# Kernel optimization log

Measured on AMD Instinct MI355X. Metric: run time of the kernel, lower is better.

The kernel has to match this reference:

```python
import jax, jax.numpy as jnp
import numpy as np
from jax import lax

B, N, L, P, C, D = 64, 20000, 336, 96, 16, 64
COARSE_K, TOPM, ALPHA, TEMP = 80, 20, 0.7, 0.1
CAT_DIM, N_TAB, GH = 16, 17, 128
ID_MIN = np.array([0,0,0,0,0,1,1,0,0,0,0,0,0,0,0,0,0], dtype=np.int64)
ID_MAX = np.array([2047,255,4095,23,6,12,53,3,1,1,15,7,2,2,2,2,1], dtype=np.int64)

def _gelu(x):
    return jax.nn.gelu(x, approximate=False)

def _mlp2(x, w1, b1, w2, b2):
    return _gelu(x @ w1 + b1) @ w2 + b2

def _ln(x, g, b):
    m = x.mean(-1, keepdims=True)
    v = jnp.var(x, axis=-1, keepdims=True)
    return (x - m) / jnp.sqrt(v + 1e-5) * g + b

def _unit(x):
    return x / (jnp.linalg.norm(x, axis=-1, keepdims=True) + 1e-12)

def setup_inputs():
    key = jax.random.key(0)
    ks = jax.random.split(key, 24)
    s = 0.02
    z = jnp.zeros
    return {
        'meta_ids': jax.random.randint(ks[0], (B, N_TAB), 0, 2),
        'exogenous_vars': jax.random.normal(ks[1], (B, 8)),
        'local_state_by_period': jax.random.normal(ks[2], (B, 3, 4)),
        'x': jax.random.normal(ks[3], (B, L, C)),
        'pool_context': jax.random.normal(ks[4], (N, D)),
        'pool_x': jax.random.normal(ks[5], (N, L, C)),
        'pool_y': jax.random.normal(ks[6], (N, P, C)),
        'emb_tables': jax.random.normal(ks[7], (N_TAB, 4096, CAT_DIM)) * s,
        'cat_w1': jax.random.normal(ks[8], (N_TAB * CAT_DIM, D)) * s, 'cat_b1': z((D,)),
        'cat_w2': jax.random.normal(ks[9], (D, D)) * s, 'cat_b2': z((D,)),
        'exo_w1': jax.random.normal(ks[10], (8, D)) * s, 'exo_b1': z((D,)),
        'exo_w2': jax.random.normal(ks[11], (D, D)) * s, 'exo_b2': z((D,)),
        'loc_w1': jax.random.normal(ks[12], (4, D)) * s, 'loc_b1': z((D,)),
        'loc_w2': jax.random.normal(ks[13], (D, D)) * s, 'loc_b2': z((D,)),
        'ln_g': jnp.ones((D,)), 'ln_b': z((D,)),
        'gate_w1': jax.random.normal(ks[14], (2 * D + 2, GH)) * s, 'gate_b1': z((GH,)),
        'gate_w2': jax.random.normal(ks[15], (GH, 1)) * s, 'gate_b2': z((1,)),
    }

def _forward(meta_ids, exogenous_vars, local_state_by_period, x, pool_context, pool_x, pool_y,
             emb_tables, cat_w1, cat_b1, cat_w2, cat_b2, exo_w1, exo_b1, exo_w2, exo_b2,
             loc_w1, loc_b1, loc_w2, loc_b2, ln_g, ln_b, gate_w1, gate_b1, gate_w2, gate_b2):
    # --- hierarchical context encoder ---
    ids = jnp.clip(meta_ids, jnp.asarray(ID_MIN)[None, :], jnp.asarray(ID_MAX)[None, :])
    # per-table embedding lookup -> [B, 17, cat_dim]
    cat = jax.vmap(lambda t, i: t[i], in_axes=(0, 1), out_axes=1)(emb_tables, ids)
    cat = cat.reshape(B, N_TAB * CAT_DIM)
    cat_ctx = _mlp2(cat, cat_w1, cat_b1, cat_w2, cat_b2)
    cat_ctx = cat_ctx + _mlp2(exogenous_vars, exo_w1, exo_b1, exo_w2, exo_b2)
    loc = _mlp2(local_state_by_period.reshape(-1, 4), loc_w1, loc_b1, loc_w2, loc_b2).reshape(B, 3, D)
    ctx = _ln(cat_ctx[:, None, :] + loc, ln_g, ln_b)       # [B, 3, D]
    q = ctx.mean(axis=1)                                    # pooled query context [B, D]
    # --- coarse retrieval: cosine sim over meta pool ---
    meta_sim = _unit(q) @ _unit(pool_context).T             # [B, N]
    meta_c, coarse_idx = lax.top_k(meta_sim, COARSE_K)      # [B, K]
    cand_ctx = pool_context[coarse_idx]                     # [B, K, D]
    cand_x = pool_x[coarse_idx]                             # [B, K, L, C]
    # --- fine similarity on raw series ---
    xf = _unit(x.reshape(B, L * C))
    cf = _unit(cand_x.reshape(B, COARSE_K, L * C))
    series_sim = jnp.einsum('bd,bkd->bk', xf, cf)
    combined = ALPHA * meta_c + (1.0 - ALPHA) * series_sim
    comb_m, li = lax.top_k(combined, TOPM)                  # [B, M]
    meta_m = jnp.take_along_axis(meta_c, li, axis=1)
    ctx_m = jnp.take_along_axis(cand_ctx, li[..., None], axis=1)   # [B, M, D]
    fin_idx = jnp.take_along_axis(coarse_idx, li, axis=1)
    cand_y = pool_y[fin_idx]                                # [B, M, P, C]
    # --- gated aggregation ---
    gate_in = jnp.concatenate([
        jnp.broadcast_to(q[:, None, :], (B, TOPM, D)), ctx_m,
        comb_m[..., None], meta_m[..., None]], axis=-1)     # [B, M, 2D+2]
    gate = _mlp2(gate_in, gate_w1, gate_b1, gate_w2, gate_b2)[..., 0]
    w = jax.nn.softmax(comb_m / TEMP + gate, axis=-1)       # [B, M]
    return jnp.einsum('bm,bmpc->bpc', w, cand_y)            # [B, P, C]

def reference(meta_ids, exogenous_vars, local_state_by_period, x, pool_context, pool_x, pool_y,
              emb_tables, cat_w1, cat_b1, cat_w2, cat_b2, exo_w1, exo_b1, exo_w2, exo_b2,
              loc_w1, loc_b1, loc_w2, loc_b2, ln_g, ln_b, gate_w1, gate_b1, gate_w2, gate_b2):
    return _forward(meta_ids, exogenous_vars, local_state_by_period, x, pool_context, pool_x, pool_y,
                    emb_tables, cat_w1, cat_b1, cat_w2, cat_b2, exo_w1, exo_b1, exo_w2, exo_b2,
                    loc_w1, loc_b1, loc_w2, loc_b2, ln_g, ln_b, gate_w1, gate_b1, gate_w2, gate_b2)
```

## Files before the change

kernel.cpp:

```cpp
#include <hip/hip_runtime.h>
#include <math.h>

typedef unsigned int u32;

#define BB 64
#define NN 20000
#define LL 336
#define PP 96
#define CC 16
#define DD 64
#define KC 80
#define TM 20
#define LC 5376
#define NTAB 17
#define GH 128
#define CAP 2048

__constant__ int c_idmin[17] = {0,0,0,0,0,1,1,0,0,0,0,0,0,0,0,0,0};
__constant__ int c_idmax[17] = {2047,255,4095,23,6,12,53,3,1,1,15,7,2,2,2,2,1};

__device__ __forceinline__ float gelu(float x){ return 0.5f*x*(1.0f + erff(x*0.70710678118654752440f)); }
__device__ __forceinline__ float wred(float v){
  #pragma unroll
  for(int m=32;m>=1;m>>=1) v += __shfl_xor(v, m, 64);
  return v;
}
__device__ __forceinline__ u32 fkey(float f){
  u32 u = __float_as_uint(f);
  return (u & 0x80000000u) ? ~u : (u | 0x80000000u);
}

#define OFF_Q     0u
#define OFF_QN    16384u
#define OFF_XN    32768u
#define OFF_CIDX  33024u
#define OFF_METC  53504u
#define OFF_COMB  73984u
#define OFF_FIDX  94464u
#define OFF_W     99584u
#define OFF_SIM   106496u

__global__ __launch_bounds__(64) void k_ctx(
    const int* __restrict__ mids, const float* __restrict__ exo,
    const float* __restrict__ locs, const float* __restrict__ x,
    const float* __restrict__ emb,
    const float* __restrict__ cw1, const float* __restrict__ cb1,
    const float* __restrict__ cw2, const float* __restrict__ cb2,
    const float* __restrict__ ew1, const float* __restrict__ eb1,
    const float* __restrict__ ew2, const float* __restrict__ eb2,
    const float* __restrict__ lw1, const float* __restrict__ lb1,
    const float* __restrict__ lw2, const float* __restrict__ lb2,
    const float* __restrict__ lng, const float* __restrict__ lnb,
    float* __restrict__ q, float* __restrict__ qn, float* __restrict__ xn)
{
  int b = blockIdx.x, j = threadIdx.x;
  __shared__ float s_cat[272];
  __shared__ float s_h[64];
  __shared__ float s_exo[8];
  __shared__ float s_loc[12];

  for(int e=j; e<272; e+=64){
    int t=e>>4, c=e&15;
    int id = mids[b*NTAB + t];
    if(id < c_idmin[t]) id = c_idmin[t];
    if(id > c_idmax[t]) id = c_idmax[t];
    s_cat[e] = emb[((size_t)t*4096 + id)*16 + c];
  }
  if(j<8)  s_exo[j] = exo[b*8+j];
  if(j<12) s_loc[j] = locs[b*12+j];
  __syncthreads();

  float a = cb1[j];
  for(int i=0;i<272;i++) a += s_cat[i]*cw1[i*64+j];
  s_h[j] = gelu(a);
  __syncthreads();
  float cc = cb2[j];
  for(int k=0;k<64;k++) cc += s_h[k]*cw2[k*64+j];
  __syncthreads();

  a = eb1[j];
  for(int i=0;i<8;i++) a += s_exo[i]*ew1[i*64+j];
  s_h[j] = gelu(a);
  __syncthreads();
  float ec = eb2[j];
  for(int k=0;k<64;k++) ec += s_h[k]*ew2[k*64+j];
  cc += ec;
  __syncthreads();

  float lr[3];
  for(int r=0;r<3;r++){
    a = lb1[j];
    for(int i=0;i<4;i++) a += s_loc[r*4+i]*lw1[i*64+j];
    s_h[j] = gelu(a);
    __syncthreads();
    float o = lb2[j];
    for(int k=0;k<64;k++) o += s_h[k]*lw2[k*64+j];
    lr[r] = o;
    __syncthreads();
  }

  float g = lng[j], be = lnb[j];
  float qa = 0.f;
  for(int r=0;r<3;r++){
    float v = cc + lr[r];
    float mean = wred(v) * (1.0f/64.0f);
    float d = v - mean;
    float var = wred(d*d) * (1.0f/64.0f);
    qa += d / sqrtf(var + 1e-5f) * g + be;
  }
  float qv = qa * (1.0f/3.0f);
  q[b*64+j] = qv;
  float s2 = wred(qv*qv);
  qn[b*64+j] = qv / (sqrtf(s2) + 1e-12f);

  float xa = 0.f;
  for(int e=j; e<LC; e+=64){ float f = x[(size_t)b*LC+e]; xa += f*f; }
  xa = wred(xa);
  if(j==0) xn[b] = sqrtf(xa);
}

__device__ __attribute__((noinline)) float row_sim(const float* pr, const float* sq)
{
  const float4* p4 = (const float4*)pr;
  float dot=0.f, ns=0.f;
  #pragma unroll
  for(int i=0;i<16;i++){
    float4 u = p4[i];
    dot += u.x*sq[i*4+0] + u.y*sq[i*4+1] + u.z*sq[i*4+2] + u.w*sq[i*4+3];
    ns  += u.x*u.x + u.y*u.y + u.z*u.z + u.w*u.w;
  }
  return dot / (sqrtf(ns) + 1e-12f);
}

__global__ __launch_bounds__(256) void k_sim(const float* __restrict__ pc,
    const float* __restrict__ qn, float* __restrict__ sim)
{
  __shared__ float s_pc[64*68];
  __shared__ float s_qn[4*64];
  int n0 = blockIdx.x << 6;
  int b0 = blockIdx.y << 2;
  int tid = threadIdx.x;

  const float4* pc4 = (const float4*)pc;
  for(int e=tid; e<64*16; e+=256){
    int r = e>>4, c = e&15;
    float4 v;
    if(n0 + r < NN) v = pc4[(size_t)(n0+r)*16 + c];
    else            v = make_float4(0.f,0.f,0.f,0.f);
    *(float4*)&s_pc[r*68 + c*4] = v;
  }
  s_qn[tid] = qn[(size_t)(b0 + (tid>>6))*64 + (tid&63)];
  __syncthreads();

  int bl = tid>>6, ln = tid&63;
  const float4* q4 = (const float4*)&s_qn[bl*64];
  const float4* p4 = (const float4*)&s_pc[ln*68];
  float dot=0.f, ns=0.f;
  #pragma unroll
  for(int i=0;i<16;i++){
    float4 p = p4[i], qv = q4[i];
    dot += p.x*qv.x + p.y*qv.y + p.z*qv.z + p.w*qv.w;
    ns  += p.x*p.x + p.y*p.y + p.z*p.z + p.w*p.w;
  }
  int n = n0 + ln;
  if(n < NN) sim[(size_t)(b0+bl)*NN + n] = dot / (sqrtf(ns) + 1e-12f);
}

__global__ __launch_bounds__(256) void k_sel(const float* __restrict__ sim,
    int* __restrict__ cidx_out, float* __restrict__ metc)
{
  __shared__ u32 hist[4096];
  __shared__ u32 cs[256];
  __shared__ float cval[CAP];
  __shared__ int  cidxs[CAP];
  __shared__ int s_T; __shared__ u32 s_above;
  __shared__ u32 s_na, s_nc;
  __shared__ float swv[4]; __shared__ int swi[4];
  int b = blockIdx.x, tid = threadIdx.x;
  const float* srow = sim + (size_t)b*NN;

  for(int e=tid;e<4096;e+=256) hist[e]=0;
  if(tid==0){ s_na=0; s_nc=0; }
  for(int e=tid;e<KC;e+=256){ cidx_out[b*KC+e]=0; metc[b*KC+e]=-1.0f; }
  __syncthreads();

  for(int n=tid;n<NN;n+=256) atomicAdd(&hist[fkey(srow[n])>>20], 1u);
  __syncthreads();
  u32 c=0;
  #pragma unroll
  for(int i=0;i<16;i++) c += hist[tid*16+i];
  cs[tid]=c;
  __syncthreads();
  if(tid==0){
    u32 acc=0, above=0; int T=0;
    for(int ch=255; ch>=0; --ch){
      if(acc + cs[ch] >= (u32)KC){
        for(int bin=ch*16+15;; --bin){
          if(acc + hist[bin] >= (u32)KC){ T=bin; above=acc; break; }
          acc += hist[bin];
        }
        break;
      }
      acc += cs[ch];
    }
    s_T = T; s_above = above;
  }
  __syncthreads();
  int T = s_T; u32 above = s_above;

  for(int n=tid;n<NN;n+=256){
    float v = srow[n];
    int k = (int)(fkey(v)>>20);
    if(k > T){
      u32 p = atomicAdd(&s_na,1u);
      if(p < (u32)KC){ cidx_out[b*KC+p] = n; metc[b*KC+p] = v; }
    } else if(k == T){
      u32 p = atomicAdd(&s_nc,1u);
      if(p < CAP){ cval[p]=v; cidxs[p]=n; }
    }
  }
  __syncthreads();
  int need = KC - (int)above; if(need < 0) need = 0;
  int Mc = (int)s_nc; if(Mc > CAP) Mc = CAP;
  for(int r=0;r<need;r++){
    float v=-3.0e38f; int i=-1;
    for(int e=tid;e<Mc;e+=256){ if(cval[e]>v){v=cval[e];i=e;} }
    int lane=tid&63, w=tid>>6;
    #pragma unroll
    for(int m=32;m>=1;m>>=1){
      float ov=__shfl_xor(v,m,64); int oi=__shfl_xor(i,m,64);
      if(ov>v){v=ov;i=oi;}
    }
    if(lane==0){ swv[w]=v; swi[w]=i; }
    __syncthreads();
    if(tid==0){
      float bv=swv[0]; int bi=swi[0];
      for(int k2=1;k2<4;k2++) if(swv[k2]>bv){bv=swv[k2];bi=swi[k2];}
      if(bi >= 0){
        cidx_out[b*KC+above+r] = cidxs[bi];
        metc[b*KC+above+r] = bv;
        cval[bi] = -3.0e38f;
      }
    }
    __syncthreads();
  }
}

__global__ __launch_bounds__(256) void k_csel(const float* __restrict__ pc,
    const float* __restrict__ qn, int* __restrict__ cidx_out, float* __restrict__ metc)
{
  __shared__ u32 hist[4096];
  __shared__ u32 cs[256];
  __shared__ float cval[CAP];
  __shared__ int  cidxs[CAP];
  __shared__ float s_qn[64];
  __shared__ int s_T; __shared__ u32 s_above;
  __shared__ u32 s_na, s_nc;
  __shared__ float swv[4]; __shared__ int swi[4];
  int b = blockIdx.x, tid = threadIdx.x;

  for(int e=tid;e<4096;e+=256) hist[e]=0;
  if(tid<64) s_qn[tid] = qn[b*64+tid];
  if(tid==0){ s_na=0; s_nc=0; }
  for(int e=tid;e<KC;e+=256){ cidx_out[b*KC+e]=0; metc[b*KC+e]=-1.0f; }
  __syncthreads();

  for(int n=tid;n<NN;n+=256){
    float v = row_sim(pc + (size_t)n*64, s_qn);
    atomicAdd(&hist[fkey(v)>>20], 1u);
  }
  __syncthreads();
  u32 c=0;
  #pragma unroll
  for(int i=0;i<16;i++) c += hist[tid*16+i];
  cs[tid]=c;
  __syncthreads();
  if(tid==0){
    u32 acc=0, above=0; int T=0;
    for(int ch=255; ch>=0; --ch){
      if(acc + cs[ch] >= (u32)KC){
        for(int bin=ch*16+15;; --bin){
          if(acc + hist[bin] >= (u32)KC){ T=bin; above=acc; break; }
          acc += hist[bin];
        }
        break;
      }
      acc += cs[ch];
    }
    s_T = T; s_above = above;
  }
  __syncthreads();
  int T = s_T; u32 above = s_above;

  for(int n=tid;n<NN;n+=256){
    float v = row_sim(pc + (size_t)n*64, s_qn);
    int k = (int)(fkey(v)>>20);
    if(k > T){
      u32 p = atomicAdd(&s_na,1u);
      if(p < (u32)KC){ cidx_out[b*KC+p] = n; metc[b*KC+p] = v; }
    } else if(k == T){
      u32 p = atomicAdd(&s_nc,1u);
      if(p < CAP){ cval[p]=v; cidxs[p]=n; }
    }
  }
  __syncthreads();
  int need = KC - (int)above; if(need < 0) need = 0;
  int Mc = (int)s_nc; if(Mc > CAP) Mc = CAP;
  for(int r=0;r<need;r++){
    float v=-3.0e38f; int i=-1;
    for(int e=tid;e<Mc;e+=256){ if(cval[e]>v){v=cval[e];i=e;} }
    int lane=tid&63, w=tid>>6;
    #pragma unroll
    for(int m=32;m>=1;m>>=1){
      float ov=__shfl_xor(v,m,64); int oi=__shfl_xor(i,m,64);
      if(ov>v){v=ov;i=oi;}
    }
    if(lane==0){ swv[w]=v; swi[w]=i; }
    __syncthreads();
    if(tid==0){
      float bv=swv[0]; int bi=swi[0];
      for(int k2=1;k2<4;k2++) if(swv[k2]>bv){bv=swv[k2];bi=swi[k2];}
      if(bi >= 0){
        cidx_out[b*KC+above+r] = cidxs[bi];
        metc[b*KC+above+r] = bv;
        cval[bi] = -3.0e38f;
      }
    }
    __syncthreads();
  }
}

__global__ __launch_bounds__(256) void k_fine(const float* __restrict__ px,
    const float* __restrict__ x, const int* __restrict__ cidx,
    const float* __restrict__ metc, const float* __restrict__ xn,
    float* __restrict__ comb)
{
  __shared__ float s_red[8];
  int blk = blockIdx.x;
  int b = blk / KC, k = blk % KC;
  int idx = cidx[b*KC+k];
  if(idx < 0) idx = 0;
  if(idx >= NN) idx = NN-1;
  const float4* pr = (const float4*)(px + (size_t)idx*LC);
  const float4* xr = (const float4*)(x + (size_t)b*LC);
  int tid = threadIdx.x;
  float dot=0.f, ns=0.f;
  for(int i=tid; i<LC/4; i+=256){
    float4 a = pr[i], cx = xr[i];
    dot += cx.x*a.x + cx.y*a.y + cx.z*a.z + cx.w*a.w;
    ns  += a.x*a.x + a.y*a.y + a.z*a.z + a.w*a.w;
  }
  dot = wred(dot); ns = wred(ns);
  int lane=tid&63, w=tid>>6;
  if(lane==0){ s_red[w]=dot; s_red[4+w]=ns; }
  __syncthreads();
  if(tid==0){
    float dd = s_red[0]+s_red[1]+s_red[2]+s_red[3];
    float nn = s_red[4]+s_red[5]+s_red[6]+s_red[7];
    float s = dd / ((xn[b]+1e-12f)*(sqrtf(nn)+1e-12f));
    comb[b*KC+k] = 0.7f*metc[b*KC+k] + (1.0f-0.7f)*s;
  }
}

__global__ __launch_bounds__(256) void k_gate(const float* __restrict__ comb,
    const float* __restrict__ metc, const int* __restrict__ cidx,
    const float* __restrict__ q, const float* __restrict__ pc,
    const float* __restrict__ gw1, const float* __restrict__ gb1,
    const float* __restrict__ gw2, const float* __restrict__ gb2,
    int* __restrict__ fidx, float* __restrict__ wout)
{
  __shared__ float s_w1[130*128];
  __shared__ float s_comb[80], s_met[80]; __shared__ int s_ci[80];
  __shared__ float s_q[64];
  __shared__ float s_ctxw[4*64];
  __shared__ float selv[20], selm[20]; __shared__ int seli[20];
  __shared__ float s_gate[20];
  __shared__ float swv2[4]; __shared__ int swi2[4];
  int b=blockIdx.x, tid=threadIdx.x;

  const float4* g4 = (const float4*)gw1;
  float4* s4 = (float4*)s_w1;
  for(int e=tid;e<4160;e+=256) s4[e] = g4[e];
  if(tid<80){
    s_comb[tid]=comb[b*KC+tid]; s_met[tid]=metc[b*KC+tid];
    int ci = cidx[b*KC+tid];
    if(ci<0) ci=0;
    if(ci>=NN) ci=NN-1;
    s_ci[tid]=ci;
  }
  if(tid<64) s_q[tid]=q[b*64+tid];
  __syncthreads();

  for(int r=0;r<TM;r++){
    float v=-3.0e38f; int i=-1;
    if(tid<80){ v=s_comb[tid]; i=tid; }
    int lane=tid&63, w=tid>>6;
    #pragma unroll
    for(int m=32;m>=1;m>>=1){
      float ov=__shfl_xor(v,m,64); int oi=__shfl_xor(i,m,64);
      if(ov>v){v=ov;i=oi;}
    }
    if(lane==0){ swv2[w]=v; swi2[w]=i; }
    __syncthreads();
    if(tid==0){
      float bv=swv2[0]; int bi=swi2[0];
      for(int k2=1;k2<4;k2++) if(swv2[k2]>bv){bv=swv2[k2];bi=swi2[k2];}
      if(bi<0) bi=0;
      selv[r]=bv; selm[r]=s_met[bi]; seli[r]=s_ci[bi];
      s_comb[bi]=-3.0e38f;
    }
    __syncthreads();
  }

  int w = tid>>6, ln = tid&63;
  for(int m=w; m<TM; m+=4){
    s_ctxw[w*64+ln] = pc[(size_t)seli[m]*64 + ln];
    float a  = gb1[ln];
    float a2 = gb1[64+ln];
    for(int i=0;i<64;i++){
      float qi = s_q[i];
      a  += qi*s_w1[i*128+ln];
      a2 += qi*s_w1[i*128+64+ln];
    }
    for(int i=0;i<64;i++){
      float ci = s_ctxw[w*64+i];
      a  += ci*s_w1[(64+i)*128+ln];
      a2 += ci*s_w1[(64+i)*128+64+ln];
    }
    a  += selv[m]*s_w1[128*128+ln];
    a  += selm[m]*s_w1[129*128+ln];
    a2 += selv[m]*s_w1[128*128+64+ln];
    a2 += selm[m]*s_w1[129*128+64+ln];
    float h = gelu(a)*gw2[ln] + gelu(a2)*gw2[64+ln];
    float s = wred(h);
    if(ln==0) s_gate[m] = s + gb2[0];
  }
  __syncthreads();

  if(tid==0){
    float lg[20]; float mx=-3.0e38f;
    for(int m=0;m<TM;m++){ lg[m] = selv[m]*10.0f + s_gate[m]; if(lg[m]>mx) mx=lg[m]; }
    float ss=0.f;
    for(int m=0;m<TM;m++){ lg[m]=expf(lg[m]-mx); ss+=lg[m]; }
    for(int m=0;m<TM;m++){ wout[b*TM+m]=lg[m]/ss; fidx[b*TM+m]=seli[m]; }
  }
}

__global__ __launch_bounds__(192) void k_out(const float* __restrict__ py,
    const int* __restrict__ fidx, const float* __restrict__ wv,
    float* __restrict__ out)
{
  __shared__ float s_w[20]; __shared__ int s_i[20];
  int b=blockIdx.x, half=blockIdx.y, tid=threadIdx.x;
  if(tid<TM){
    s_w[tid]=wv[b*TM+tid];
    int ii=fidx[b*TM+tid];
    if(ii<0) ii=0;
    if(ii>=NN) ii=NN-1;
    s_i[tid]=ii;
  }
  __syncthreads();
  int e4 = half*192 + tid;
  const float4* py4 = (const float4*)py;
  float4 acc = make_float4(0.f,0.f,0.f,0.f);
  #pragma unroll
  for(int m=0;m<TM;m++){
    float4 v = py4[(size_t)s_i[m]*(PP*CC/4) + e4];
    float wm = s_w[m];
    acc.x += wm*v.x; acc.y += wm*v.y; acc.z += wm*v.z; acc.w += wm*v.w;
  }
  ((float4*)out)[(size_t)b*(PP*CC/4) + e4] = acc;
}

extern "C" void kernel_launch(void* const* d_in, const int* in_sizes, int n_in,
                              void* d_out, int out_size, void* d_ws, size_t ws_size,
                              hipStream_t stream) {
  const int*   mids = (const int*)d_in[0];
  const float* exo  = (const float*)d_in[1];
  const float* locs = (const float*)d_in[2];
  const float* x    = (const float*)d_in[3];
  const float* pc   = (const float*)d_in[4];
  const float* px   = (const float*)d_in[5];
  const float* py   = (const float*)d_in[6];
  const float* emb  = (const float*)d_in[7];
  const float* cw1  = (const float*)d_in[8];
  const float* cb1  = (const float*)d_in[9];
  const float* cw2  = (const float*)d_in[10];
  const float* cb2  = (const float*)d_in[11];
  const float* ew1  = (const float*)d_in[12];
  const float* eb1  = (const float*)d_in[13];
  const float* ew2  = (const float*)d_in[14];
  const float* eb2  = (const float*)d_in[15];
  const float* lw1  = (const float*)d_in[16];
  const float* lb1  = (const float*)d_in[17];
  const float* lw2  = (const float*)d_in[18];
  const float* lb2  = (const float*)d_in[19];
  const float* lng  = (const float*)d_in[20];
  const float* lnb  = (const float*)d_in[21];
  const float* gw1  = (const float*)d_in[22];
  const float* gb1  = (const float*)d_in[23];
  const float* gw2  = (const float*)d_in[24];
  const float* gb2  = (const float*)d_in[25];
  float* out = (float*)d_out;

  char* ws = (char*)d_ws;
  float* q    = (float*)(ws + OFF_Q);
  float* qn   = (float*)(ws + OFF_QN);
  float* xn   = (float*)(ws + OFF_XN);
  int*   cidx = (int*)  (ws + OFF_CIDX);
  float* metc = (float*)(ws + OFF_METC);
  float* comb = (float*)(ws + OFF_COMB);
  int*   fidx = (int*)  (ws + OFF_FIDX);
  float* wv   = (float*)(ws + OFF_W);
  float* sims = (float*)(ws + OFF_SIM);

  k_ctx<<<BB, 64, 0, stream>>>(mids, exo, locs, x, emb,
      cw1, cb1, cw2, cb2, ew1, eb1, ew2, eb2,
      lw1, lb1, lw2, lb2, lng, lnb, q, qn, xn);

  size_t need_sim = (size_t)OFF_SIM + (size_t)BB*NN*sizeof(float);
  if(ws_size >= need_sim){
    k_sim<<<dim3((NN+63)/64, BB/4), 256, 0, stream>>>(pc, qn, sims);
    k_sel<<<BB, 256, 0, stream>>>(sims, cidx, metc);
  } else {
    k_csel<<<BB, 256, 0, stream>>>(pc, qn, cidx, metc);
  }

  k_fine<<<BB*KC, 256, 0, stream>>>(px, x, cidx, metc, xn, comb);
  k_gate<<<BB, 256, 0, stream>>>(comb, metc, cidx, q, pc,
      gw1, gb1, gw2, gb2, fidx, wv);
  k_out<<<dim3(BB,2), 192, 0, stream>>>(py, fidx, wv, out);
}
```

Before: 781.9 us.

## Add second radix-histogram pass to top-K selection and vectorize sim reads

The top-K selection kernel now runs a second 12-bit histogram pass over the boundary-bin candidates. This narrows how many elements need the serial argmax loop, which previously ran up to `need` block-wide reductions with syncthreads. The sim row is also read as float4. The extra histogram pass adds shared-memory clears and atomics, but it should cut the per-rank reduction iterations sharply.

```diff
diff --git a/kernel.cpp b/kernel.cpp
--- a/kernel.cpp
+++ b/kernel.cpp
@@ -174,17 +174,25 @@
   __shared__ float cval[CAP];
   __shared__ int  cidxs[CAP];
   __shared__ int s_T; __shared__ u32 s_above;
-  __shared__ u32 s_na, s_nc;
+  __shared__ int s_T2; __shared__ u32 s_above2;
+  __shared__ u32 s_na, s_nc, s_nb;
   __shared__ float swv[4]; __shared__ int swi[4];
   int b = blockIdx.x, tid = threadIdx.x;
   const float* srow = sim + (size_t)b*NN;
+  const float4* srow4 = (const float4*)srow;
 
   for(int e=tid;e<4096;e+=256) hist[e]=0;
-  if(tid==0){ s_na=0; s_nc=0; }
+  if(tid==0){ s_na=0; s_nc=0; s_nb=0; }
   for(int e=tid;e<KC;e+=256){ cidx_out[b*KC+e]=0; metc[b*KC+e]=-1.0f; }
   __syncthreads();
 
-  for(int n=tid;n<NN;n+=256) atomicAdd(&hist[fkey(srow[n])>>20], 1u);
+  for(int i=tid;i<NN/4;i+=256){
+    float4 v = srow4[i];
+    atomicAdd(&hist[fkey(v.x)>>20], 1u);
+    atomicAdd(&hist[fkey(v.y)>>20], 1u);
+    atomicAdd(&hist[fkey(v.z)>>20], 1u);
+    atomicAdd(&hist[fkey(v.w)>>20], 1u);
+  }
   __syncthreads();
   u32 c=0;
   #pragma unroll
@@ -208,21 +216,71 @@
   __syncthreads();
   int T = s_T; u32 above = s_above;
 
-  for(int n=tid;n<NN;n+=256){
-    float v = srow[n];
-    int k = (int)(fkey(v)>>20);
-    if(k > T){
-      u32 p = atomicAdd(&s_na,1u);
-      if(p < (u32)KC){ cidx_out[b*KC+p] = n; metc[b*KC+p] = v; }
-    } else if(k == T){
-      u32 p = atomicAdd(&s_nc,1u);
-      if(p < CAP){ cval[p]=v; cidxs[p]=n; }
+  for(int i=tid;i<NN/4;i+=256){
+    float4 vv = srow4[i];
+    float va[4] = {vv.x, vv.y, vv.z, vv.w};
+    #pragma unroll
+    for(int cix=0;cix<4;cix++){
+      float v = va[cix];
+      int k = (int)(fkey(v)>>20);
+      if(k > T){
+        u32 p = atomicAdd(&s_na,1u);
+        if(p < (u32)KC){ int n = i*4+cix; cidx_out[b*KC+p] = n; metc[b*KC+p] = v; }
+      } else if(k == T){
+        u32 p = atomicAdd(&s_nc,1u);
+        if(p < CAP){ cval[p]=v; cidxs[p]=i*4+cix; }
+      }
     }
   }
   __syncthreads();
   int need = KC - (int)above; if(need < 0) need = 0;
   int Mc = (int)s_nc; if(Mc > CAP) Mc = CAP;
-  for(int r=0;r<need;r++){
+
+  for(int e=tid;e<4096;e+=256) hist[e]=0;
+  __syncthreads();
+  for(int e=tid;e<Mc;e+=256) atomicAdd(&hist[(fkey(cval[e])>>8)&0xFFFu], 1u);
+  __syncthreads();
+  u32 c2=0;
+  #pragma unroll
+  for(int i=0;i<16;i++) c2 += hist[tid*16+i];
+  cs[tid]=c2;
+  __syncthreads();
+  if(tid==0){
+    if(need == 0){ s_T2 = 4096; s_above2 = 0; }
+    else {
+      u32 acc=0, above2=0; int T2=0;
+      for(int ch=255; ch>=0; --ch){
+        if(acc + cs[ch] >= (u32)need){
+          for(int bin=ch*16+15;; --bin){
+            if(acc + hist[bin] >= (u32)need){ T2=bin; above2=acc; break; }
+            acc += hist[bin];
+          }
+          break;
+        }
+        acc += cs[ch];
+      }
+      s_T2 = T2; s_above2 = above2;
+    }
+  }
+  __syncthreads();
+  int T2 = s_T2; u32 above2 = s_above2;
+
+  for(int e=tid;e<Mc;e+=256){
+    float v = cval[e];
+    int sub = (int)((fkey(v)>>8)&0xFFFu);
+    if(sub > T2){
+      u32 p = atomicAdd(&s_nb,1u);
+      if(p < (u32)need){
+        cidx_out[b*KC+above+p] = cidxs[e];
+        metc[b*KC+above+p] = v;
+      }
+      cval[e] = -3.0e38f;
+    }
+  }
+  __syncthreads();
+
+  int need2 = need - (int)above2; if(need2 < 0) need2 = 0;
+  for(int r=0;r<need2;r++){
     float v=-3.0e38f; int i=-1;
     for(int e=tid;e<Mc;e+=256){ if(cval[e]>v){v=cval[e];i=e;} }
     int lane=tid&63, w=tid>>6;
@@ -237,8 +295,8 @@
       float bv=swv[0]; int bi=swi[0];
       for(int k2=1;k2<4;k2++) if(swv[k2]>bv){bv=swv[k2];bi=swi[k2];}
       if(bi >= 0){
-        cidx_out[b*KC+above+r] = cidxs[bi];
-        metc[b*KC+above+r] = bv;
+        cidx_out[b*KC+above+above2+r] = cidxs[bi];
+        metc[b*KC+above+above2+r] = bv;
         cval[bi] = -3.0e38f;
       }
     }
```

Result: faster. 754.9 us (-3.4%).
